# Kernel tuning notes

Measured on AMD Instinct MI355X. Metric: run time of the kernel, lower is better.

The kernel has to match this reference:

```python
import jax, jax.numpy as jnp
import numpy as np

P = 3           # planes (u, v, y)
N = 50000       # nodes per plane
E = 256000      # edges per plane
C = 5           # num_classes
F_IN, F_NODE, F_EDGE = 4, 64, 16
F = F_IN + F_NODE  # 68, per-node feature dim


def setup_inputs() -> dict:
    key = jax.random.key(0)
    ks = jax.random.split(key, 10)
    s = 0.05  # weight scale for numerical sanity
    return {
        "x": jax.random.normal(ks[0], (P, N, C, F), jnp.float32),
        "edge_index": jax.random.randint(ks[1], (P, 2, E), 0, N, dtype=jnp.int64),
        "We1": jax.random.normal(ks[2], (P, C, F_EDGE, 2 * F), jnp.float32) * s,
        "be1": jax.random.normal(ks[3], (P, C, F_EDGE), jnp.float32) * s,
        "We2": jax.random.normal(ks[4], (P, C, 1, F_EDGE), jnp.float32) * s,
        "be2": jax.random.normal(ks[5], (P, C, 1), jnp.float32) * s,
        "Wn1": jax.random.normal(ks[6], (P, C, F_NODE, 2 * F), jnp.float32) * s,
        "bn1": jax.random.normal(ks[7], (P, C, F_NODE), jnp.float32) * s,
        "Wn2": jax.random.normal(ks[8], (P, C, F_NODE, F_NODE), jnp.float32) * s,
        "bn2": jax.random.normal(ks[9], (P, C, F_NODE), jnp.float32) * s,
    }


def class_linear(x, W, b):
    # x: [n, C, fin], W: [C, fout, fin], b: [C, fout] -> [n, C, fout]
    return jnp.einsum('ncf,cgf->ncg', x, W) + b


def mp_plane(x, ei, We1, be1, We2, be2, Wn1, bn1, Wn2, bn2):
    # MessagePassing2D (source_to_target): x_j = source, x_i = target
    src, dst = ei[0], ei[1]
    x_i = x[dst]                                # [E, C, F]
    x_j = x[src]                                # [E, C, F]
    # edge_net input is detached in the original (stop_gradient)
    m_in = jax.lax.stop_gradient(jnp.concatenate([x_i, x_j], axis=-1))  # [E, C, 2F]
    h = jnp.tanh(class_linear(m_in, We1, be1))  # [E, C, F_EDGE]
    logits = class_linear(h, We2, be2)          # [E, C, 1]
    w = jax.nn.softmax(logits, axis=1)          # softmax over class dim (dim=1)
    msg = w * x_j                               # [E, C, F]
    aggr = jax.ops.segment_sum(msg, dst, num_segments=N)  # scatter-add to targets
    u_in = jnp.concatenate([x, aggr], axis=-1)  # [N, C, 2F]
    h2 = jnp.tanh(class_linear(u_in, Wn1, bn1))
    return jnp.tanh(class_linear(h2, Wn2, bn2))  # [N, C, F_NODE]


def reference(x, edge_index, We1, be1, We2, be2, Wn1, bn1, Wn2, bn2):
    # vmap over the 3 detector planes (PlaneNet ModuleDict)
    return jax.vmap(mp_plane)(x, edge_index, We1, be1, We2, be2,
                              Wn1, bn1, Wn2, bn2)  # [P, N, C, F_NODE]
```

## Files before the change

### kernel.cpp

```cpp
#include <hip/hip_runtime.h>
#include <hip/hip_fp16.h>
#include <math.h>

constexpr int kP  = 3;
constexpr int kN  = 50000;
constexpr int kE  = 256000;
constexpr int kC  = 5;
constexpr int kF  = 68;
constexpr int kF2 = 136;
constexpr int kFE = 16;
constexpr int kFN = 64;
constexpr int kOfsStride = 50004;

__device__ __forceinline__ float fast_tanh(float x) {
  float t = fminf(fmaxf(x, -15.f), 15.f);
  float e = __expf(2.f * t);
  return (e - 1.f) / (e + 1.f);
}

__global__ __launch_bounds__(256) void hist_kernel(
    const int* __restrict__ ei,
    int* __restrict__ counts)
{
  int p = blockIdx.y;
  int e = blockIdx.x * 256 + threadIdx.x;
  if (e >= kE) return;
  int dst = ei[(size_t)p * 2 * kE + kE + e];
  atomicAdd(&counts[p * kN + dst], 1);
}

__global__ __launch_bounds__(1024) void scan_kernel(
    const int* __restrict__ counts,
    int* __restrict__ offsets,
    int* __restrict__ cursor)
{
  int p = blockIdx.x;
  const int* cnt = counts + p * kN;
  int* ofs = offsets + p * kOfsStride;
  int* cur = cursor + p * kN;
  __shared__ int buf[1024];
  __shared__ int carry_s;
  int tid = threadIdx.x;
  if (tid == 0) carry_s = 0;
  __syncthreads();
  for (int base = 0; base < kN; base += 1024) {
    int i = base + tid;
    int v = (i < kN) ? cnt[i] : 0;
    buf[tid] = v;
    __syncthreads();
    for (int d = 1; d < 1024; d <<= 1) {
      int t = (tid >= d) ? buf[tid - d] : 0;
      __syncthreads();
      buf[tid] += t;
      __syncthreads();
    }
    int incl = buf[tid];
    int carry = carry_s;
    if (i < kN) {
      int excl = carry + incl - v;
      ofs[i] = excl;
      cur[i] = excl;
    }
    __syncthreads();
    if (tid == 1023) carry_s = carry + incl;
    __syncthreads();
  }
  if (tid == 0) ofs[kN] = carry_s;
}

__global__ __launch_bounds__(256) void pre_kernel(
    const float* __restrict__ x,
    const float* __restrict__ We1,
    float* __restrict__ yi,
    float* __restrict__ yj)
{
  int n = blockIdx.x * 256 + threadIdx.x;
  int c = blockIdx.y;
  if (n >= kN) return;

  const float4* xr = reinterpret_cast<const float4*>(x + ((size_t)n * kC + c) * kF);
  const float* Wc = We1 + c * (kFE * kF2);

  float ai[kFE], aj[kFE];
#pragma unroll
  for (int g = 0; g < kFE; ++g) { ai[g] = 0.f; aj[g] = 0.f; }

  for (int q = 0; q < kF / 4; ++q) {
    float4 v = xr[q];
#pragma unroll
    for (int g = 0; g < kFE; ++g) {
      const float* wi = Wc + g * kF2 + 4 * q;
      const float* wj = wi + kF;
      float a = ai[g];
      a = fmaf(wi[0], v.x, a); a = fmaf(wi[1], v.y, a);
      a = fmaf(wi[2], v.z, a); a = fmaf(wi[3], v.w, a);
      ai[g] = a;
      float b = aj[g];
      b = fmaf(wj[0], v.x, b); b = fmaf(wj[1], v.y, b);
      b = fmaf(wj[2], v.z, b); b = fmaf(wj[3], v.w, b);
      aj[g] = b;
    }
  }

  float4* oi = reinterpret_cast<float4*>(yi + ((size_t)n * kC + c) * kFE);
  float4* oj = reinterpret_cast<float4*>(yj + ((size_t)n * kC + c) * kFE);
#pragma unroll
  for (int k = 0; k < 4; ++k) {
    oi[k] = make_float4(ai[4*k], ai[4*k+1], ai[4*k+2], ai[4*k+3]);
    oj[k] = make_float4(aj[4*k], aj[4*k+1], aj[4*k+2], aj[4*k+3]);
  }
}

__global__ __launch_bounds__(256) void pre_z_kernel(
    const float* __restrict__ x,
    const float* __restrict__ Wn1,
    __half* __restrict__ z)
{
  int n = blockIdx.x * 256 + threadIdx.x;
  int c = blockIdx.y;
  if (n >= kN) return;

  float4 xr[kF / 4];
  const float4* xp = reinterpret_cast<const float4*>(x + ((size_t)n * kC + c) * kF);
#pragma unroll
  for (int q = 0; q < kF / 4; ++q) xr[q] = xp[q];

  const float* W = Wn1 + c * (kFN * kF2) + kF;
  uint4* zp = reinterpret_cast<uint4*>(z + ((size_t)n * kC + c) * kFN);

  for (int g0 = 0; g0 < kFN; g0 += 8) {
    float acc[8];
#pragma unroll
    for (int t = 0; t < 8; ++t) acc[t] = 0.f;
#pragma unroll
    for (int q = 0; q < kF / 4; ++q) {
      float4 v = xr[q];
#pragma unroll
      for (int t = 0; t < 8; ++t) {
        const float* wr = W + (size_t)(g0 + t) * kF2 + 4 * q;
        float a = acc[t];
        a = fmaf(wr[0], v.x, a); a = fmaf(wr[1], v.y, a);
        a = fmaf(wr[2], v.z, a); a = fmaf(wr[3], v.w, a);
        acc[t] = a;
      }
    }
    __half2 p0 = __floats2half2_rn(acc[0], acc[1]);
    __half2 p1 = __floats2half2_rn(acc[2], acc[3]);
    __half2 p2 = __floats2half2_rn(acc[4], acc[5]);
    __half2 p3 = __floats2half2_rn(acc[6], acc[7]);
    uint4 pk;
    pk.x = *reinterpret_cast<unsigned int*>(&p0);
    pk.y = *reinterpret_cast<unsigned int*>(&p1);
    pk.z = *reinterpret_cast<unsigned int*>(&p2);
    pk.w = *reinterpret_cast<unsigned int*>(&p3);
    zp[g0 >> 3] = pk;
  }
}

__global__ __launch_bounds__(256) void edge_kernel(
    const int*   __restrict__ ei,
    const float* __restrict__ yi,
    const float* __restrict__ yj,
    const float* __restrict__ be1,
    const float* __restrict__ We2,
    const float* __restrict__ be2,
    int*         __restrict__ cursor,
    int*         __restrict__ sorted_src,
    float*       __restrict__ w_sorted)
{
  int e = blockIdx.x * 256 + threadIdx.x;
  if (e >= kE) return;
  int src = ei[e];
  int dst = ei[kE + e];

  const float* yid = yi + (size_t)dst * (kC * kFE);
  const float* yjs = yj + (size_t)src * (kC * kFE);

  float logits[kC];
#pragma unroll
  for (int c = 0; c < kC; ++c) {
    const float4* a = reinterpret_cast<const float4*>(yid + c * kFE);
    const float4* b = reinterpret_cast<const float4*>(yjs + c * kFE);
    float lg = be2[c];
#pragma unroll
    for (int qq = 0; qq < 4; ++qq) {
      float4 av = a[qq];
      float4 bv = b[qq];
      const float* bb = be1 + c * kFE + 4 * qq;
      const float* w2 = We2 + c * kFE + 4 * qq;
      lg = fmaf(w2[0], fast_tanh(av.x + bv.x + bb[0]), lg);
      lg = fmaf(w2[1], fast_tanh(av.y + bv.y + bb[1]), lg);
      lg = fmaf(w2[2], fast_tanh(av.z + bv.z + bb[2]), lg);
      lg = fmaf(w2[3], fast_tanh(av.w + bv.w + bb[3]), lg);
    }
    logits[c] = lg;
  }

  float m = logits[0];
#pragma unroll
  for (int c = 1; c < kC; ++c) m = fmaxf(m, logits[c]);
  float wgt[kC];
  float s = 0.f;
#pragma unroll
  for (int c = 0; c < kC; ++c) { wgt[c] = __expf(logits[c] - m); s += wgt[c]; }
  float inv = 1.f / s;

  int pos = atomicAdd(&cursor[dst], 1);
  sorted_src[pos] = src;
#pragma unroll
  for (int c = 0; c < kC; ++c) w_sorted[(size_t)pos * kC + c] = wgt[c] * inv;
}

__global__ __launch_bounds__(256) void node_kernel(
    const float*  __restrict__ x,
    const int*    __restrict__ offsets,
    const int*    __restrict__ sorted_src,
    const float*  __restrict__ w_sorted,
    const __half* __restrict__ z,
    const float*  __restrict__ Wn1,
    const float*  __restrict__ bn1,
    const float*  __restrict__ Wn2,
    const float*  __restrict__ bn2,
    float*        __restrict__ out)
{
  int n = blockIdx.x * 256 + threadIdx.x;
  int c = blockIdx.y;
  if (n >= kN) return;

  int beg = offsets[n];
  int end = offsets[n + 1];

  float h[kFN];
#pragma unroll
  for (int g = 0; g < kFN; ++g) h[g] = 0.f;

  for (int s = beg; s < end; ++s) {
    int sj = sorted_src[s];
    float w = w_sorted[(size_t)s * kC + c];
    const uint4* zp = reinterpret_cast<const uint4*>(z + ((size_t)sj * kC + c) * kFN);
#pragma unroll
    for (int u = 0; u < 8; ++u) {
      uint4 v = zp[u];
      float2 f0 = __half22float2(*reinterpret_cast<const __half2*>(&v.x));
      float2 f1 = __half22float2(*reinterpret_cast<const __half2*>(&v.y));
      float2 f2 = __half22float2(*reinterpret_cast<const __half2*>(&v.z));
      float2 f3 = __half22float2(*reinterpret_cast<const __half2*>(&v.w));
      h[8*u+0] = fmaf(w, f0.x, h[8*u+0]);
      h[8*u+1] = fmaf(w, f0.y, h[8*u+1]);
      h[8*u+2] = fmaf(w, f1.x, h[8*u+2]);
      h[8*u+3] = fmaf(w, f1.y, h[8*u+3]);
      h[8*u+4] = fmaf(w, f2.x, h[8*u+4]);
      h[8*u+5] = fmaf(w, f2.y, h[8*u+5]);
      h[8*u+6] = fmaf(w, f3.x, h[8*u+6]);
      h[8*u+7] = fmaf(w, f3.y, h[8*u+7]);
    }
  }

  const float* W1 = Wn1 + c * (kFN * kF2);
  const float4* xp = reinterpret_cast<const float4*>(x + ((size_t)n * kC + c) * kF);
  for (int q = 0; q < kF / 4; ++q) {
    float4 v = xp[q];
#pragma unroll
    for (int g = 0; g < kFN; ++g) {
      const float* wr = W1 + (size_t)g * kF2 + 4 * q;
      float a = h[g];
      a = fmaf(wr[0], v.x, a);
      a = fmaf(wr[1], v.y, a);
      a = fmaf(wr[2], v.z, a);
      a = fmaf(wr[3], v.w, a);
      h[g] = a;
    }
  }

  const float* b1 = bn1 + c * kFN;
#pragma unroll
  for (int g = 0; g < kFN; ++g) h[g] = fast_tanh(h[g] + b1[g]);

  const float* W2 = Wn2 + c * (kFN * kFN);
  const float* b2 = bn2 + c * kFN;
  float4* op = reinterpret_cast<float4*>(out + ((size_t)n * kC + c) * kFN);
  for (int g2 = 0; g2 < kFN; g2 += 4) {
    float a0 = b2[g2], a1 = b2[g2 + 1], a2 = b2[g2 + 2], a3 = b2[g2 + 3];
    const float* w0 = W2 + (size_t)g2 * kFN;
#pragma unroll
    for (int k = 0; k < kFN; ++k) {
      float hk = h[k];
      a0 = fmaf(w0[k],            hk, a0);
      a1 = fmaf(w0[kFN + k],      hk, a1);
      a2 = fmaf(w0[2 * kFN + k],  hk, a2);
      a3 = fmaf(w0[3 * kFN + k],  hk, a3);
    }
    op[g2 >> 2] = make_float4(fast_tanh(a0), fast_tanh(a1),
                              fast_tanh(a2), fast_tanh(a3));
  }
}

extern "C" void kernel_launch(void* const* d_in, const int* in_sizes, int n_in,
                              void* d_out, int out_size, void* d_ws, size_t ws_size,
                              hipStream_t stream) {
  const float* x   = (const float*)d_in[0];
  const int*   ei  = (const int*)  d_in[1];
  const float* We1 = (const float*)d_in[2];
  const float* be1 = (const float*)d_in[3];
  const float* We2 = (const float*)d_in[4];
  const float* be2 = (const float*)d_in[5];
  const float* Wn1 = (const float*)d_in[6];
  const float* bn1 = (const float*)d_in[7];
  const float* Wn2 = (const float*)d_in[8];
  const float* bn2 = (const float*)d_in[9];
  float* out = (float*)d_out;

  int* counts  = (int*)d_ws;
  int* offsets = counts + kP * kN;
  int* cursor  = offsets + kP * kOfsStride;
  int* sorted_src = cursor + kP * kN;
  float* w_sorted = (float*)(sorted_src + kE);
  float* yi = w_sorted + (size_t)kE * kC;
  float* yj = yi + (size_t)kN * kC * kFE;
  __half* z = (__half*)yi;

  const size_t planeX = (size_t)kN * kC * kF;

  hipMemsetAsync(counts, 0, (size_t)kP * kN * sizeof(int), stream);
  hist_kernel<<<dim3(kE / 256, kP), 256, 0, stream>>>(ei, counts);
  scan_kernel<<<kP, 1024, 0, stream>>>(counts, offsets, cursor);

  for (int p = 0; p < kP; ++p) {
    const float* xp = x + p * planeX;

    pre_kernel<<<dim3((kN + 255) / 256, kC), 256, 0, stream>>>(
        xp, We1 + (size_t)p * kC * kFE * kF2, yi, yj);

    edge_kernel<<<kE / 256, 256, 0, stream>>>(
        ei + (size_t)p * 2 * kE, yi, yj,
        be1 + (size_t)p * kC * kFE,
        We2 + (size_t)p * kC * kFE,
        be2 + (size_t)p * kC,
        cursor + p * kN, sorted_src, w_sorted);

    pre_z_kernel<<<dim3((kN + 255) / 256, kC), 256, 0, stream>>>(
        xp, Wn1 + (size_t)p * kC * kFN * kF2, z);

    node_kernel<<<dim3((kN + 255) / 256, kC), 256, 0, stream>>>(
        xp, offsets + p * kOfsStride, sorted_src, w_sorted, z,
        Wn1 + (size_t)p * kC * kFN * kF2,
        bn1 + (size_t)p * kC * kFN,
        Wn2 + (size_t)p * kC * kFN * kFN,
        bn2 + (size_t)p * kC * kFN,
        out + (size_t)p * kN * kC * kFN);
  }
}
```

Baseline: 1.939 ms.

## Parallelize offset scan across blocks and split node MLP across thread pairs

Replaces the single-block-per-plane serial scan with a three-phase multi-block scan (chunk scan, partials scan, add-back). The node kernel now assigns two threads per node, each computing half of the hidden and output features. The hidden activations are exchanged through shared memory as fp16 for the second layer. This lowers register pressure and raises parallelism, at the cost of duplicated edge loops and index reads plus extra fp16 rounding of the hidden layer.

```diff
diff --git a/kernel.cpp b/kernel.cpp
--- a/kernel.cpp
+++ b/kernel.cpp
@@ -11,6 +11,8 @@
 constexpr int kFE = 16;
 constexpr int kFN = 64;
 constexpr int kOfsStride = 50004;
+constexpr int kNChunks = (kN + 1023) / 1024;
+constexpr int kPartStride = 64;
 
 __device__ __forceinline__ float fast_tanh(float x) {
   float t = fminf(fmaxf(x, -15.f), 15.f);
@@ -29,43 +31,88 @@
   atomicAdd(&counts[p * kN + dst], 1);
 }
 
-__global__ __launch_bounds__(1024) void scan_kernel(
+__global__ __launch_bounds__(256) void scanA_kernel(
     const int* __restrict__ counts,
     int* __restrict__ offsets,
+    int* __restrict__ partials)
+{
+  int p = blockIdx.y, chunk = blockIdx.x, tid = threadIdx.x;
+  const int* cnt = counts + p * kN;
+  int base = chunk * 1024 + tid * 4;
+  int v0 = 0, v1 = 0, v2 = 0, v3 = 0;
+  if (base + 3 < kN) {
+    int4 v = *reinterpret_cast<const int4*>(cnt + base);
+    v0 = v.x; v1 = v.y; v2 = v.z; v3 = v.w;
+  } else if (base < kN) {
+    v0 = cnt[base];
+    if (base + 1 < kN) v1 = cnt[base + 1];
+    if (base + 2 < kN) v2 = cnt[base + 2];
+  }
+  int s0 = v0, s1 = s0 + v1, s2 = s1 + v2, s3 = s2 + v3;
+  __shared__ int buf[256];
+  buf[tid] = s3;
+  __syncthreads();
+  for (int d = 1; d < 256; d <<= 1) {
+    int t = (tid >= d) ? buf[tid - d] : 0;
+    __syncthreads();
+    buf[tid] += t;
+    __syncthreads();
+  }
+  int excl = buf[tid] - s3;
+  int* ofs = offsets + p * kOfsStride;
+  if (base + 3 < kN) {
+    *reinterpret_cast<int4*>(ofs + base) =
+        make_int4(excl, excl + s0, excl + s1, excl + s2);
+  } else if (base < kN) {
+    ofs[base] = excl;
+    if (base + 1 < kN) ofs[base + 1] = excl + s0;
+    if (base + 2 < kN) ofs[base + 2] = excl + s1;
+  }
+  if (tid == 255) partials[p * kPartStride + chunk] = buf[255];
+}
+
+__global__ __launch_bounds__(64) void scanB_kernel(int* __restrict__ partials)
+{
+  int p = blockIdx.x, tid = threadIdx.x;
+  int v = (tid < kNChunks) ? partials[p * kPartStride + tid] : 0;
+  __shared__ int buf[64];
+  buf[tid] = v;
+  __syncthreads();
+  for (int d = 1; d < 64; d <<= 1) {
+    int t = (tid >= d) ? buf[tid - d] : 0;
+    __syncthreads();
+    buf[tid] += t;
+    __syncthreads();
+  }
+  partials[p * kPartStride + tid] = buf[tid] - v;
+}
+
+__global__ __launch_bounds__(256) void scanC_kernel(
+    int* __restrict__ offsets,
+    const int* __restrict__ partials,
     int* __restrict__ cursor)
 {
-  int p = blockIdx.x;
-  const int* cnt = counts + p * kN;
+  int p = blockIdx.y, chunk = blockIdx.x, tid = threadIdx.x;
+  int add = partials[p * kPartStride + chunk];
+  int base = chunk * 1024 + tid * 4;
   int* ofs = offsets + p * kOfsStride;
   int* cur = cursor + p * kN;
-  __shared__ int buf[1024];
-  __shared__ int carry_s;
-  int tid = threadIdx.x;
-  if (tid == 0) carry_s = 0;
-  __syncthreads();
-  for (int base = 0; base < kN; base += 1024) {
-    int i = base + tid;
-    int v = (i < kN) ? cnt[i] : 0;
-    buf[tid] = v;
-    __syncthreads();
-    for (int d = 1; d < 1024; d <<= 1) {
-      int t = (tid >= d) ? buf[tid - d] : 0;
-      __syncthreads();
-      buf[tid] += t;
-      __syncthreads();
-    }
-    int incl = buf[tid];
-    int carry = carry_s;
-    if (i < kN) {
-      int excl = carry + incl - v;
-      ofs[i] = excl;
-      cur[i] = excl;
-    }
-    __syncthreads();
-    if (tid == 1023) carry_s = carry + incl;
-    __syncthreads();
-  }
-  if (tid == 0) ofs[kN] = carry_s;
+  if (base + 3 < kN) {
+    int4 v = *reinterpret_cast<const int4*>(ofs + base);
+    v.x += add; v.y += add; v.z += add; v.w += add;
+    *reinterpret_cast<int4*>(ofs + base) = v;
+    *reinterpret_cast<int4*>(cur + base) = v;
+  } else if (base < kN) {
+#pragma unroll
+    for (int k = 0; k < 3; ++k) {
+      if (base + k < kN) {
+        int o = ofs[base + k] + add;
+        ofs[base + k] = o;
+        cur[base + k] = o;
+      }
+    }
+  }
+  if (chunk == 0 && tid == 0) ofs[kN] = partials[p * kPartStride + kNChunks];
 }
 
 __global__ __launch_bounds__(256) void pre_kernel(
@@ -211,7 +258,7 @@
   for (int c = 0; c < kC; ++c) w_sorted[(size_t)pos * kC + c] = wgt[c] * inv;
 }
 
-__global__ __launch_bounds__(256) void node_kernel(
+__global__ __launch_bounds__(256) void node_pair_kernel(
     const float*  __restrict__ x,
     const int*    __restrict__ offsets,
     const int*    __restrict__ sorted_src,
@@ -223,75 +270,130 @@
     const float*  __restrict__ bn2,
     float*        __restrict__ out)
 {
-  int n = blockIdx.x * 256 + threadIdx.x;
+  __shared__ __align__(16) unsigned char hsm[128 * 144];
+  int tid = threadIdx.x;
+  int i = blockIdx.x * 256 + tid;
+  int n = i >> 1;
+  int half = i & 1;
   int c = blockIdx.y;
-  if (n >= kN) return;
-
-  int beg = offsets[n];
-  int end = offsets[n + 1];
-
-  float h[kFN];
-#pragma unroll
-  for (int g = 0; g < kFN; ++g) h[g] = 0.f;
-
-  for (int s = beg; s < end; ++s) {
-    int sj = sorted_src[s];
-    float w = w_sorted[(size_t)s * kC + c];
-    const uint4* zp = reinterpret_cast<const uint4*>(z + ((size_t)sj * kC + c) * kFN);
-#pragma unroll
-    for (int u = 0; u < 8; ++u) {
-      uint4 v = zp[u];
-      float2 f0 = __half22float2(*reinterpret_cast<const __half2*>(&v.x));
-      float2 f1 = __half22float2(*reinterpret_cast<const __half2*>(&v.y));
-      float2 f2 = __half22float2(*reinterpret_cast<const __half2*>(&v.z));
-      float2 f3 = __half22float2(*reinterpret_cast<const __half2*>(&v.w));
-      h[8*u+0] = fmaf(w, f0.x, h[8*u+0]);
-      h[8*u+1] = fmaf(w, f0.y, h[8*u+1]);
-      h[8*u+2] = fmaf(w, f1.x, h[8*u+2]);
-      h[8*u+3] = fmaf(w, f1.y, h[8*u+3]);
-      h[8*u+4] = fmaf(w, f2.x, h[8*u+4]);
-      h[8*u+5] = fmaf(w, f2.y, h[8*u+5]);
-      h[8*u+6] = fmaf(w, f3.x, h[8*u+6]);
-      h[8*u+7] = fmaf(w, f3.y, h[8*u+7]);
-    }
-  }
-
-  const float* W1 = Wn1 + c * (kFN * kF2);
-  const float4* xp = reinterpret_cast<const float4*>(x + ((size_t)n * kC + c) * kF);
-  for (int q = 0; q < kF / 4; ++q) {
-    float4 v = xp[q];
-#pragma unroll
-    for (int g = 0; g < kFN; ++g) {
-      const float* wr = W1 + (size_t)g * kF2 + 4 * q;
-      float a = h[g];
-      a = fmaf(wr[0], v.x, a);
-      a = fmaf(wr[1], v.y, a);
-      a = fmaf(wr[2], v.z, a);
-      a = fmaf(wr[3], v.w, a);
-      h[g] = a;
-    }
-  }
-
-  const float* b1 = bn1 + c * kFN;
-#pragma unroll
-  for (int g = 0; g < kFN; ++g) h[g] = fast_tanh(h[g] + b1[g]);
-
-  const float* W2 = Wn2 + c * (kFN * kFN);
-  const float* b2 = bn2 + c * kFN;
-  float4* op = reinterpret_cast<float4*>(out + ((size_t)n * kC + c) * kFN);
-  for (int g2 = 0; g2 < kFN; g2 += 4) {
-    float a0 = b2[g2], a1 = b2[g2 + 1], a2 = b2[g2 + 2], a3 = b2[g2 + 3];
-    const float* w0 = W2 + (size_t)g2 * kFN;
-#pragma unroll
-    for (int k = 0; k < kFN; ++k) {
-      float hk = h[k];
-      a0 = fmaf(w0[k],            hk, a0);
-      a1 = fmaf(w0[kFN + k],      hk, a1);
-      a2 = fmaf(w0[2 * kFN + k],  hk, a2);
-      a3 = fmaf(w0[3 * kFN + k],  hk, a3);
-    }
-    op[g2 >> 2] = make_float4(fast_tanh(a0), fast_tanh(a1),
-                              fast_tanh(a2), fast_tanh(a3));
+  bool active = (n < kN);
+  int pr = tid >> 1;
+
+  if (active) {
+    int beg = offsets[n];
+    int end = offsets[n + 1];
+
+    float h[32];
+#pragma unroll
+    for (int g = 0; g < 32; ++g) h[g] = 0.f;
+
+    for (int s = beg; s < end; ++s) {
+      int sj = sorted_src[s];
+      float w = w_sorted[(size_t)s * kC + c];
+      const uint4* zp = reinterpret_cast<const uint4*>(
+          z + ((size_t)sj * kC + c) * kFN + half * 32);
+#pragma unroll
+      for (int u = 0; u < 4; ++u) {
+        uint4 v = zp[u];
+        float2 f0 = __half22float2(*reinterpret_cast<const __half2*>(&v.x));
+        float2 f1 = __half22float2(*reinterpret_cast<const __half2*>(&v.y));
+        float2 f2 = __half22float2(*reinterpret_cast<const __half2*>(&v.z));
+        float2 f3 = __half22float2(*reinterpret_cast<const __half2*>(&v.w));
+        h[8*u+0] = fmaf(w, f0.x, h[8*u+0]);
+        h[8*u+1] = fmaf(w, f0.y, h[8*u+1]);
+        h[8*u+2] = fmaf(w, f1.x, h[8*u+2]);
+        h[8*u+3] = fmaf(w, f1.y, h[8*u+3]);
+        h[8*u+4] = fmaf(w, f2.x, h[8*u+4]);
+        h[8*u+5] = fmaf(w, f2.y, h[8*u+5]);
+        h[8*u+6] = fmaf(w, f3.x, h[8*u+6]);
+        h[8*u+7] = fmaf(w, f3.y, h[8*u+7]);
+      }
+    }
+
+    const float* W1 = Wn1 + c * (kFN * kF2) + (size_t)(half * 32) * kF2;
+    const float4* xp = reinterpret_cast<const float4*>(x + ((size_t)n * kC + c) * kF);
+    for (int q = 0; q < kF / 4; ++q) {
+      float4 v = xp[q];
+#pragma unroll
+      for (int j = 0; j < 32; ++j) {
+        const float* wr = W1 + (size_t)j * kF2 + 4 * q;
+        float a = h[j];
+        a = fmaf(wr[0], v.x, a);
+        a = fmaf(wr[1], v.y, a);
+        a = fmaf(wr[2], v.z, a);
+        a = fmaf(wr[3], v.w, a);
+        h[j] = a;
+      }
+    }
+
+    const float* b1 = bn1 + c * kFN + half * 32;
+#pragma unroll
+    for (int j = 0; j < 32; ++j) h[j] = fast_tanh(h[j] + b1[j]);
+
+    uint4* wp = reinterpret_cast<uint4*>(hsm + pr * 144 + half * 64);
+#pragma unroll
+    for (int u = 0; u < 4; ++u) {
+      __half2 a = __floats2half2_rn(h[8*u+0], h[8*u+1]);
+      __half2 b = __floats2half2_rn(h[8*u+2], h[8*u+3]);
+      __half2 d = __floats2half2_rn(h[8*u+4], h[8*u+5]);
+      __half2 e = __floats2half2_rn(h[8*u+6], h[8*u+7]);
+      uint4 pk;
+      pk.x = *reinterpret_cast<unsigned int*>(&a);
+      pk.y = *reinterpret_cast<unsigned int*>(&b);
+      pk.z = *reinterpret_cast<unsigned int*>(&d);
+      pk.w = *reinterpret_cast<unsigned int*>(&e);
+      wp[u] = pk;
+    }
+  }
+
+  __syncthreads();
+  if (!active) return;
+
+  const float* W2 = Wn2 + c * (kFN * kFN) + (size_t)(half * 32) * kFN;
+  const float* b2 = bn2 + c * kFN + half * 32;
+  float* op = out + ((size_t)n * kC + c) * kFN + half * 32;
+  const uint4* hp = reinterpret_cast<const uint4*>(hsm + pr * 144);
+
+  for (int jb = 0; jb < 32; jb += 16) {
+    float acc[16];
+#pragma unroll
+    for (int j = 0; j < 16; ++j) acc[j] = b2[jb + j];
+#pragma unroll
+    for (int q = 0; q < 4; ++q) {
+      uint4 hv0 = hp[2 * q];
+      uint4 hv1 = hp[2 * q + 1];
+      float f[16];
+      const __half2* h0 = reinterpret_cast<const __half2*>(&hv0);
+      const __half2* h1 = reinterpret_cast<const __half2*>(&hv1);
+#pragma unroll
+      for (int t = 0; t < 4; ++t) {
+        float2 ff = __half22float2(h0[t]);
+        f[2*t]   = ff.x;
+        f[2*t+1] = ff.y;
+        float2 gg = __half22float2(h1[t]);
+        f[8+2*t]   = gg.x;
+        f[8+2*t+1] = gg.y;
+      }
+#pragma unroll
+      for (int j = 0; j < 16; ++j) {
+        const float* wr = W2 + (size_t)(jb + j) * kFN + q * 16;
+        float a = acc[j];
+        a = fmaf(wr[0],  f[0],  a);  a = fmaf(wr[1],  f[1],  a);
+        a = fmaf(wr[2],  f[2],  a);  a = fmaf(wr[3],  f[3],  a);
+        a = fmaf(wr[4],  f[4],  a);  a = fmaf(wr[5],  f[5],  a);
+        a = fmaf(wr[6],  f[6],  a);  a = fmaf(wr[7],  f[7],  a);
+        a = fmaf(wr[8],  f[8],  a);  a = fmaf(wr[9],  f[9],  a);
+        a = fmaf(wr[10], f[10], a);  a = fmaf(wr[11], f[11], a);
+        a = fmaf(wr[12], f[12], a);  a = fmaf(wr[13], f[13], a);
+        a = fmaf(wr[14], f[14], a);  a = fmaf(wr[15], f[15], a);
+        acc[j] = a;
+      }
+    }
+    float4* o4 = reinterpret_cast<float4*>(op + jb);
+#pragma unroll
+    for (int u = 0; u < 4; ++u)
+      o4[u] = make_float4(fast_tanh(acc[4*u]),   fast_tanh(acc[4*u+1]),
+                          fast_tanh(acc[4*u+2]), fast_tanh(acc[4*u+3]));
   }
 }
 
@@ -313,7 +415,8 @@
   int* counts  = (int*)d_ws;
   int* offsets = counts + kP * kN;
   int* cursor  = offsets + kP * kOfsStride;
-  int* sorted_src = cursor + kP * kN;
+  int* partials = cursor + kP * kN;
+  int* sorted_src = partials + kP * kPartStride;
   float* w_sorted = (float*)(sorted_src + kE);
   float* yi = w_sorted + (size_t)kE * kC;
   float* yj = yi + (size_t)kN * kC * kFE;
@@ -323,7 +426,9 @@
 
   hipMemsetAsync(counts, 0, (size_t)kP * kN * sizeof(int), stream);
   hist_kernel<<<dim3(kE / 256, kP), 256, 0, stream>>>(ei, counts);
-  scan_kernel<<<kP, 1024, 0, stream>>>(counts, offsets, cursor);
+  scanA_kernel<<<dim3(kNChunks, kP), 256, 0, stream>>>(counts, offsets, partials);
+  scanB_kernel<<<kP, 64, 0, stream>>>(partials);
+  scanC_kernel<<<dim3(kNChunks, kP), 256, 0, stream>>>(offsets, partials, cursor);
 
   for (int p = 0; p < kP; ++p) {
     const float* xp = x + p * planeX;
@@ -341,7 +446,7 @@
     pre_z_kernel<<<dim3((kN + 255) / 256, kC), 256, 0, stream>>>(
         xp, Wn1 + (size_t)p * kC * kFN * kF2, z);
 
-    node_kernel<<<dim3((kN + 255) / 256, kC), 256, 0, stream>>>(
+    node_pair_kernel<<<dim3((2 * kN + 255) / 256, kC), 256, 0, stream>>>(
         xp, offsets + p * kOfsStride, sorted_src, w_sorted, z,
         Wn1 + (size_t)p * kC * kFN * kF2,
         bn1 + (size_t)p * kC * kFN,
```

Result: slower. 2.713 ms (+39.9%).
